# Performance work log

Measured on AMD Instinct MI355X. Metric: run time of the kernel, lower is better.

## Reference

```python
import jax, jax.numpy as jnp
import numpy as np

# 25 anchors (YOLOv2 VOC anchors replicated at 5 scales) -> pred channels = 25*5 = 125
_BASE = np.array([[1.3221, 1.73145], [3.19275, 4.00944], [5.05587, 8.09892],
                  [9.47112, 4.84053], [11.2364, 10.0071]], dtype=np.float32)
ANCHORS = jnp.asarray(np.concatenate([_BASE * s for s in (0.5, 0.75, 1.0, 1.25, 1.5)], axis=0))  # (25, 2)
NUM_ANCHORS = 25
OBJECT_SCALE = 5.0
NO_OBJECT_SCALE = 1.0
COORD_SCALE = 1.0
SIL_THRESH = 0.6


def _bbox_iou(x1, y1, w1, h1, x2, y2, w2, h2):
    """IoU of center-format boxes (cx, cy, w, h); broadcasts."""
    mx = jnp.minimum(x1 - w1 * 0.5, x2 - w2 * 0.5)
    Mx = jnp.maximum(x1 + w1 * 0.5, x2 + w2 * 0.5)
    my = jnp.minimum(y1 - h1 * 0.5, y2 - h2 * 0.5)
    My = jnp.maximum(y1 + h1 * 0.5, y2 + h2 * 0.5)
    cw = w1 + w2 - (Mx - mx)
    ch = h1 + h2 - (My - my)
    inter = jnp.where((cw > 0) & (ch > 0), cw * ch, 0.0)
    union = w1 * h1 + w2 * h2 - inter
    return inter / union


def setup_inputs() -> dict:
    key = jax.random.key(0)
    k1, k2 = jax.random.split(key)
    B, C, H, W = 512, NUM_ANCHORS * 5, 38, 38
    pred = jax.random.normal(k1, (B, C, H, W), dtype=jnp.float32)
    target = jax.random.uniform(k2, (B, 4), dtype=jnp.float32)  # normalized gx, gy, gw, gh
    return {"pred": pred, "target": target, "train_out": 0}


def reference(pred, target, train_out):
    B = pred.shape[0]
    H = pred.shape[2]
    W = pred.shape[3]
    A = NUM_ANCHORS
    p = pred.reshape(B, A, 5, H, W)

    # activations (these carry gradient in the original)
    txy = jax.nn.sigmoid(p[:, :, :2])          # (B,A,2,H,W)
    twh = p[:, :, 2:4]                         # (B,A,2,H,W)
    pred_conf = jax.nn.sigmoid(p[:, :, 4])     # (B,A,H,W)

    grid_x = jnp.arange(W, dtype=jnp.float32)[None, None, None, :]
    grid_y = jnp.arange(H, dtype=jnp.float32)[None, None, :, None]
    aw = ANCHORS[:, 0][None, :, None, None]
    ah = ANCHORS[:, 1][None, :, None, None]

    # decoded boxes are detached in the original (clone().detach())
    bx = txy[:, :, 0] + grid_x
    by = txy[:, :, 1] + grid_y
    bw = jnp.exp(twh[:, :, 0]) * aw
    bh = jnp.exp(twh[:, :, 1]) * ah
    pred_boxes = jax.lax.stop_gradient(jnp.stack([bx, by, bw, bh], axis=2))  # (B,A,4,H,W)

    tgt = jax.lax.stop_gradient(target)
    gx = tgt[:, 0] * W
    gy = tgt[:, 1] * H
    gw = tgt[:, 2] * W
    gh = tgt[:, 3] * H

    # conf_mask: zero where any pred box overlaps gt above sil_thresh
    ious = _bbox_iou(pred_boxes[:, :, 0], pred_boxes[:, :, 1], pred_boxes[:, :, 2], pred_boxes[:, :, 3],
                     gx[:, None, None, None], gy[:, None, None, None],
                     gw[:, None, None, None], gh[:, None, None, None])  # (B,A,H,W)
    conf_mask = jnp.where(ious > SIL_THRESH, 0.0, NO_OBJECT_SCALE)

    # best anchor per gt by wh-only IoU
    a_iou = _bbox_iou(0.0, 0.0, ANCHORS[:, 0][None, :], ANCHORS[:, 1][None, :],
                      0.0, 0.0, gw[:, None], gh[:, None])  # (B,A)
    best = jnp.argmax(a_iou, axis=1)  # (B,)

    gi = gx.astype(jnp.int32)
    gj = gy.astype(jnp.int32)
    bidx = jnp.arange(B)
    best_aw = ANCHORS[best, 0]
    best_ah = ANCHORS[best, 1]

    # seen < 12800 branch: coord_mask all ones, target xy default 0.5
    coord_mask = jnp.ones((B, A, H, W), dtype=jnp.float32)
    target_box = jnp.zeros((B, A, 4, H, W), dtype=jnp.float32).at[:, :, :2].set(0.5)
    target_box = target_box.at[bidx, best, 0, gj, gi].set(gx - gi)
    target_box = target_box.at[bidx, best, 1, gj, gi].set(gy - gj)
    target_box = target_box.at[bidx, best, 2, gj, gi].set(jnp.log(gw / best_aw))
    target_box = target_box.at[bidx, best, 3, gj, gi].set(jnp.log(gh / best_ah))
    conf_mask = conf_mask.at[bidx, best, gj, gi].set(OBJECT_SCALE)

    pb = pred_boxes[bidx, best, :, gj, gi]  # (B,4) pred box at gt cell
    tconf = _bbox_iou(pb[:, 0], pb[:, 1], pb[:, 2], pb[:, 3], gx, gy, gw, gh)
    target_conf = jnp.zeros((B, A, H, W), dtype=jnp.float32).at[bidx, best, gj, gi].set(tconf)

    conf_mask = jnp.sqrt(conf_mask)

    def mse_sum(a, b):
        return jnp.sum((a - b) ** 2)

    loss_x = COORD_SCALE * mse_sum(txy[:, :, 0] * coord_mask, target_box[:, :, 0] * coord_mask) / 2.0
    loss_y = COORD_SCALE * mse_sum(txy[:, :, 1] * coord_mask, target_box[:, :, 1] * coord_mask) / 2.0
    loss_w = COORD_SCALE * mse_sum(twh[:, :, 0] * coord_mask, target_box[:, :, 2] * coord_mask) / 2.0
    loss_h = COORD_SCALE * mse_sum(twh[:, :, 1] * coord_mask, target_box[:, :, 3] * coord_mask) / 2.0
    loss_conf = mse_sum(pred_conf * conf_mask, target_conf * conf_mask) / 2.0
    loss = loss_x + loss_y + loss_w + loss_h + loss_conf

    if train_out:
        return (loss, loss_x, loss_y, loss_w, loss_h, loss_conf)
    return loss
```

## Files before the change

kernel.cpp:

```cpp
#include <hip/hip_runtime.h>
#include <math.h>

#define GW 38
#define GH 38
#define NA 25
#define NB 512
#define HW (GW * GH)
#define S4 (HW / 4)
#define PLANES (NB * NA)
#define HALF_PLANES (PLANES / 2)
#define T_TOTAL (HALF_PLANES * S4)
#define BLK 256

struct Meta {
    float gxlo, gxhi, gylo, gyhi;
    float gw, gh, area;
    float tconf, tb0, tb1, tb2, tb3;
    int   best, cell;
};

__device__ __forceinline__ float fast_rcp(float x) { return __builtin_amdgcn_rcpf(x); }
__device__ __forceinline__ float fast_exp(float x) { return __expf(x); }
__device__ __forceinline__ float fast_sig(float x) { return fast_rcp(1.0f + fast_exp(-x)); }

__device__ __forceinline__ float iou_precise(float x1, float y1, float w1, float h1,
                                             float x2, float y2, float w2, float h2) {
    float mx = fminf(x1 - w1 * 0.5f, x2 - w2 * 0.5f);
    float Mx = fmaxf(x1 + w1 * 0.5f, x2 + w2 * 0.5f);
    float my = fminf(y1 - h1 * 0.5f, y2 - h2 * 0.5f);
    float My = fmaxf(y1 + h1 * 0.5f, y2 + h2 * 0.5f);
    float cw = w1 + w2 - (Mx - mx);
    float ch = h1 + h2 - (My - my);
    float inter = (cw > 0.0f && ch > 0.0f) ? cw * ch : 0.0f;
    float uni = w1 * h1 + w2 * h2 - inter;
    return inter / uni;
}

__device__ __forceinline__ void anchor_wh(int a, float* aw, float* ah) {
    const float bw[5] = {1.3221f, 3.19275f, 5.05587f, 9.47112f, 11.2364f};
    const float bh[5] = {1.73145f, 4.00944f, 8.09892f, 4.84053f, 10.0071f};
    float s = 0.5f + 0.25f * (float)(a / 5);
    *aw = bw[a % 5] * s;
    *ah = bh[a % 5] * s;
}

__global__ void meta_kernel(const float* __restrict__ pred,
                            const float* __restrict__ target,
                            Meta* __restrict__ metas) {
    int b = blockIdx.x * blockDim.x + threadIdx.x;
    if (b >= NB) return;
    float gx = target[b * 4 + 0] * (float)GW;
    float gy = target[b * 4 + 1] * (float)GH;
    float gw = target[b * 4 + 2] * (float)GW;
    float gh = target[b * 4 + 3] * (float)GH;
    int best = 0;
    float best_iou = -1.0f;
    for (int a = 0; a < NA; ++a) {
        float aw, ah;
        anchor_wh(a, &aw, &ah);
        float v = iou_precise(0.0f, 0.0f, aw, ah, 0.0f, 0.0f, gw, gh);
        if (v > best_iou) { best_iou = v; best = a; }
    }
    int gi = (int)gx;
    int gj = (int)gy;
    float aw, ah;
    anchor_wh(best, &aw, &ah);
    size_t base = (size_t)b * NA * 5 * HW + (size_t)(best * 5) * HW + gj * GW + gi;
    float p0 = pred[base + 0 * HW];
    float p1 = pred[base + 1 * HW];
    float p2 = pred[base + 2 * HW];
    float p3 = pred[base + 3 * HW];
    float pbx = 1.0f / (1.0f + expf(-p0)) + (float)gi;
    float pby = 1.0f / (1.0f + expf(-p1)) + (float)gj;
    float pbw = expf(p2) * aw;
    float pbh = expf(p3) * ah;
    Meta m;
    m.gxlo = gx - gw * 0.5f; m.gxhi = gx + gw * 0.5f;
    m.gylo = gy - gh * 0.5f; m.gyhi = gy + gh * 0.5f;
    m.gw = gw; m.gh = gh; m.area = gw * gh;
    m.tconf = iou_precise(pbx, pby, pbw, pbh, gx, gy, gw, gh);
    m.tb0 = gx - (float)gi;
    m.tb1 = gy - (float)gj;
    m.tb2 = logf(gw / aw);
    m.tb3 = logf(gh / ah);
    m.best = best;
    m.cell = gj * GW + gi;
    metas[b] = m;
}

__device__ __forceinline__ float cell_loss(float p0, float p1, float p2, float p3, float p4,
                                           float fi, float fj, bool obj,
                                           const Meta& m, float aw, float ah) {
    float tx = fast_sig(p0);
    float ty = fast_sig(p1);
    float conf = fast_sig(p4);
    float bw = fast_exp(p2) * aw;
    float bh = fast_exp(p3) * ah;
    float bx = tx + fi;
    float by = ty + fj;
    float mx = fminf(bx - bw * 0.5f, m.gxlo);
    float Mx = fmaxf(bx + bw * 0.5f, m.gxhi);
    float my = fminf(by - bh * 0.5f, m.gylo);
    float My = fmaxf(by + bh * 0.5f, m.gyhi);
    float cw = bw + m.gw - (Mx - mx);
    float ch = bh + m.gh - (My - my);
    float inter = (cw > 0.0f && ch > 0.0f) ? cw * ch : 0.0f;
    float uni = bw * bh + m.area - inter;
    float iou = inter * fast_rcp(uni);
    float cm = obj ? 2.23606797749979f : ((iou > 0.6f) ? 0.0f : 1.0f);
    float dx = tx - (obj ? m.tb0 : 0.5f);
    float dy = ty - (obj ? m.tb1 : 0.5f);
    float dw = p2 - (obj ? m.tb2 : 0.0f);
    float dh = p3 - (obj ? m.tb3 : 0.0f);
    float dc = cm * (conf - (obj ? m.tconf : 0.0f));
    return dx * dx + dy * dy + dw * dw + dh * dh + dc * dc;
}

__global__ __launch_bounds__(BLK) void loss_kernel(const float* __restrict__ pred,
                                                   const Meta* __restrict__ metas,
                                                   float* __restrict__ out) {
    unsigned t = blockIdx.x * (unsigned)BLK + threadIdx.x;
    unsigned plane = t / (unsigned)S4;
    unsigned s4 = t - plane * (unsigned)S4;
    unsigned b = plane / (unsigned)NA;
    unsigned a = plane - b * (unsigned)NA;

    const float4* base0 = (const float4*)(pred + (size_t)plane * 5u * (unsigned)HW);
    const float4* base1 = base0 + (size_t)HALF_PLANES * 5u * (unsigned)S4;

    float4 q0 = base0[s4 + 0u * S4];
    float4 q1 = base0[s4 + 1u * S4];
    float4 q2 = base0[s4 + 2u * S4];
    float4 q3 = base0[s4 + 3u * S4];
    float4 q4 = base0[s4 + 4u * S4];
    float4 r0 = base1[s4 + 0u * S4];
    float4 r1 = base1[s4 + 1u * S4];
    float4 r2 = base1[s4 + 2u * S4];
    float4 r3 = base1[s4 + 3u * S4];
    float4 r4 = base1[s4 + 4u * S4];

    Meta m0 = metas[b];
    Meta m1 = metas[b + 256];
    float aw, ah;
    anchor_wh((int)a, &aw, &ah);
    bool aok0 = (a == (unsigned)m0.best);
    bool aok1 = (a == (unsigned)m1.best);

    float qa[5][4] = {{q0.x, q0.y, q0.z, q0.w}, {q1.x, q1.y, q1.z, q1.w},
                      {q2.x, q2.y, q2.z, q2.w}, {q3.x, q3.y, q3.z, q3.w},
                      {q4.x, q4.y, q4.z, q4.w}};
    float ra[5][4] = {{r0.x, r0.y, r0.z, r0.w}, {r1.x, r1.y, r1.z, r1.w},
                      {r2.x, r2.y, r2.z, r2.w}, {r3.x, r3.y, r3.z, r3.w},
                      {r4.x, r4.y, r4.z, r4.w}};

    float acc = 0.0f;
#pragma unroll
    for (int k = 0; k < 4; ++k) {
        unsigned s = s4 * 4u + (unsigned)k;
        unsigned j = s / (unsigned)GW;
        unsigned i = s - j * (unsigned)GW;
        float fi = (float)i, fj = (float)j;
        bool obj0 = aok0 && (s == (unsigned)m0.cell);
        bool obj1 = aok1 && (s == (unsigned)m1.cell);
        acc += cell_loss(qa[0][k], qa[1][k], qa[2][k], qa[3][k], qa[4][k], fi, fj, obj0, m0, aw, ah);
        acc += cell_loss(ra[0][k], ra[1][k], ra[2][k], ra[3][k], ra[4][k], fi, fj, obj1, m1, aw, ah);
    }

    for (int off = 32; off > 0; off >>= 1)
        acc += __shfl_down(acc, off, 64);
    __shared__ float sm[BLK / 64];
    int lane = (int)(threadIdx.x & 63u);
    int wv = (int)(threadIdx.x >> 6u);
    if (lane == 0) sm[wv] = acc;
    __syncthreads();
    if (threadIdx.x == 0) {
        float s = sm[0] + sm[1] + sm[2] + sm[3];
        atomicAdd(out, 0.5f * s);
    }
}

extern "C" void kernel_launch(void* const* d_in, const int* in_sizes, int n_in,
                              void* d_out, int out_size, void* d_ws, size_t ws_size,
                              hipStream_t stream) {
    const float* pred = (const float*)d_in[0];
    const float* target = (const float*)d_in[1];
    float* out = (float*)d_out;
    Meta* metas = (Meta*)d_ws;

    hipMemsetAsync(d_out, 0, (size_t)out_size * sizeof(float), stream);
    meta_kernel<<<(NB + BLK - 1) / BLK, BLK, 0, stream>>>(pred, target, metas);
    loss_kernel<<<T_TOTAL / BLK, BLK, 0, stream>>>(pred, metas, out);
}
```

Before: 508.5 us.

## Stage each anchor plane in LDS with one block per plane

```diff
diff --git a/kernel.cpp b/kernel.cpp
--- a/kernel.cpp
+++ b/kernel.cpp
@@ -6,10 +6,9 @@
 #define NA 25
 #define NB 512
 #define HW (GW * GH)
-#define S4 (HW / 4)
-#define PLANES (NB * NA)
-#define HALF_PLANES (PLANES / 2)
-#define T_TOTAL (HALF_PLANES * S4)
+#define PLANE_F (5 * HW)
+#define PLANE_V (PLANE_F / 4)
+#define NBLOCKS (NB * NA)
 #define BLK 256
 
 struct Meta {
@@ -119,51 +118,42 @@
 __global__ __launch_bounds__(BLK) void loss_kernel(const float* __restrict__ pred,
                                                    const Meta* __restrict__ metas,
                                                    float* __restrict__ out) {
-    unsigned t = blockIdx.x * (unsigned)BLK + threadIdx.x;
-    unsigned plane = t / (unsigned)S4;
-    unsigned s4 = t - plane * (unsigned)S4;
+    __shared__ float4 lds4[PLANE_V];
+    float* lds = (float*)lds4;
+
+    unsigned plane = blockIdx.x;
     unsigned b = plane / (unsigned)NA;
     unsigned a = plane - b * (unsigned)NA;
 
-    const float4* base0 = (const float4*)(pred + (size_t)plane * 5u * (unsigned)HW);
-    const float4* base1 = base0 + (size_t)HALF_PLANES * 5u * (unsigned)S4;
+    const float4* src = (const float4*)(pred + (size_t)plane * (unsigned)PLANE_F);
+#pragma unroll
+    for (int r = 0; r < 8; ++r) {
+        unsigned idx = threadIdx.x + (unsigned)(r * BLK);
+        if (idx < (unsigned)PLANE_V) lds4[idx] = src[idx];
+    }
 
-    float4 q0 = base0[s4 + 0u * S4];
-    float4 q1 = base0[s4 + 1u * S4];
-    float4 q2 = base0[s4 + 2u * S4];
-    float4 q3 = base0[s4 + 3u * S4];
-    float4 q4 = base0[s4 + 4u * S4];
-    float4 r0 = base1[s4 + 0u * S4];
-    float4 r1 = base1[s4 + 1u * S4];
-    float4 r2 = base1[s4 + 2u * S4];
-    float4 r3 = base1[s4 + 3u * S4];
-    float4 r4 = base1[s4 + 4u * S4];
-
-    Meta m0 = metas[b];
-    Meta m1 = metas[b + 256];
+    Meta m = metas[b];
     float aw, ah;
     anchor_wh((int)a, &aw, &ah);
-    bool aok0 = (a == (unsigned)m0.best);
-    bool aok1 = (a == (unsigned)m1.best);
+    bool aok = (a == (unsigned)m.best);
 
-    float qa[5][4] = {{q0.x, q0.y, q0.z, q0.w}, {q1.x, q1.y, q1.z, q1.w},
-                      {q2.x, q2.y, q2.z, q2.w}, {q3.x, q3.y, q3.z, q3.w},
-                      {q4.x, q4.y, q4.z, q4.w}};
-    float ra[5][4] = {{r0.x, r0.y, r0.z, r0.w}, {r1.x, r1.y, r1.z, r1.w},
-                      {r2.x, r2.y, r2.z, r2.w}, {r3.x, r3.y, r3.z, r3.w},
-                      {r4.x, r4.y, r4.z, r4.w}};
+    __syncthreads();
 
     float acc = 0.0f;
 #pragma unroll
-    for (int k = 0; k < 4; ++k) {
-        unsigned s = s4 * 4u + (unsigned)k;
-        unsigned j = s / (unsigned)GW;
-        unsigned i = s - j * (unsigned)GW;
-        float fi = (float)i, fj = (float)j;
-        bool obj0 = aok0 && (s == (unsigned)m0.cell);
-        bool obj1 = aok1 && (s == (unsigned)m1.cell);
-        acc += cell_loss(qa[0][k], qa[1][k], qa[2][k], qa[3][k], qa[4][k], fi, fj, obj0, m0, aw, ah);
-        acc += cell_loss(ra[0][k], ra[1][k], ra[2][k], ra[3][k], ra[4][k], fi, fj, obj1, m1, aw, ah);
+    for (int r = 0; r < 6; ++r) {
+        unsigned s = threadIdx.x + (unsigned)(r * BLK);
+        if (s < (unsigned)HW) {
+            float p0 = lds[0 * HW + s];
+            float p1 = lds[1 * HW + s];
+            float p2 = lds[2 * HW + s];
+            float p3 = lds[3 * HW + s];
+            float p4 = lds[4 * HW + s];
+            unsigned j = s / (unsigned)GW;
+            unsigned i = s - j * (unsigned)GW;
+            bool obj = aok && (s == (unsigned)m.cell);
+            acc += cell_loss(p0, p1, p2, p3, p4, (float)i, (float)j, obj, m, aw, ah);
+        }
     }
 
     for (int off = 32; off > 0; off >>= 1)
@@ -189,5 +179,5 @@
 
     hipMemsetAsync(d_out, 0, (size_t)out_size * sizeof(float), stream);
     meta_kernel<<<(NB + BLK - 1) / BLK, BLK, 0, stream>>>(pred, target, metas);
-    loss_kernel<<<T_TOTAL / BLK, BLK, 0, stream>>>(pred, metas, out);
+    loss_kernel<<<NBLOCKS, BLK, 0, stream>>>(pred, metas, out);
 }
```

Result: slower. 560.2 us (+10.2%).
